# Kernel tuning notes

Hardware: AMD Instinct MI355X
Metric: run time of the kernel (lower is better)

Reference implementation:

```python
import jax, jax.numpy as jnp
import numpy as np

N_NODES = 50000
N_EDGES = 800000
D_FEAT = 96
HIDDEN = 96
AVG_DEG = 16.0


def setup_inputs() -> dict:
    key = jax.random.key(0)
    k1, k2, k3, k4, k5 = jax.random.split(key, 5)
    x = jax.random.normal(k1, (N_NODES, D_FEAT), dtype=jnp.float32)
    row = jax.random.randint(k2, (N_EDGES,), 0, N_NODES)
    col = jax.random.randint(k3, (N_EDGES,), 0, N_NODES)
    edge_index = jnp.stack([row, col]).astype(jnp.int32)  # [2, E]
    # normalized adjacency values ~ 1/degree scale
    edge_weight = jax.random.uniform(k4, (N_EDGES,), dtype=jnp.float32) / AVG_DEG
    # init_w: small normal + identity (random=False path)
    W = 0.1 * jax.random.normal(k5, (D_FEAT, HIDDEN), dtype=jnp.float32) + jnp.eye(D_FEAT, HIDDEN, dtype=jnp.float32)
    b = jnp.zeros((HIDDEN,), dtype=jnp.float32)
    return {"x": x, "W": W, "b": b, "edge_index": edge_index, "edge_weight": edge_weight}


def reference(x, W, b, edge_index, edge_weight):
    # dense projection + bias
    h = x @ W + b  # [N, H]
    # sparse adj matmul: out[i] = sum_e w_e * h[col_e] for row_e == i
    row, col = edge_index[0], edge_index[1]
    msgs = edge_weight[:, None] * h[col]  # [E, H]
    pre_nonlinearity = jax.ops.segment_sum(msgs, row, num_segments=N_NODES)  # [N, H]
    # inference path: no dropout (training=None)
    output = jax.nn.elu(pre_nonlinearity)
    return (pre_nonlinearity, output)
```

## Files before the change

### kernel.cpp

```cpp
#include <hip/hip_runtime.h>


#define D 96
#define CG 24
#define BSHIFT 6
#define BROWS 64
#define CAP 1536
#define CPAD 16
#define EB_CHUNK 3200
#define GR 64
#define XPITCH 25

typedef unsigned long long u64;
typedef unsigned short u16;
typedef unsigned int u32;

__device__ __forceinline__ u16 f2bf(float f) {
  const u32 u = __float_as_uint(f);
  return (u16)((u + 0x7FFFu + ((u >> 16) & 1u)) >> 16);
}
__device__ __forceinline__ float bf2f(u16 s) {
  return __uint_as_float(((u32)s) << 16);
}

struct ushort4_t { u16 x, y, z, w; };

__global__ __launch_bounds__(256) void init_bcur_kernel(int* __restrict__ bcur, int nbkt) {
  const int b = blockIdx.x * 256 + threadIdx.x;
  if (b < nbkt) bcur[b * CPAD] = b * CAP;
}

union FusedSmem {
  float4 sX[GR * XPITCH];
  struct { int cnt[1024]; int cur[1024]; } bz;
};

__global__ __launch_bounds__(256) void fused_gemm_bucketize(
    const float* __restrict__ x, const float4* __restrict__ W4,
    const float* __restrict__ bias, u16* __restrict__ h16, int n_nodes,
    const int* __restrict__ rows, const int* __restrict__ cols,
    const float* __restrict__ ew, int* __restrict__ bcur,
    u64* __restrict__ tmp, int n_edges, int nbkt, int bb) {
  __shared__ FusedSmem sm;
  const int tid = threadIdx.x;

  if ((int)blockIdx.x < bb) {
    for (int i = tid; i < 1024; i += 256) sm.bz.cnt[i] = 0;
    __syncthreads();
    const int e0 = blockIdx.x * EB_CHUNK;
    const int e1 = min(e0 + EB_CHUNK, n_edges);
    for (int e = e0 + tid; e < e1; e += 256)
      atomicAdd(&sm.bz.cnt[rows[e] >> BSHIFT], 1);
    __syncthreads();
    for (int b = tid; b < nbkt; b += 256) {
      const int c = sm.bz.cnt[b];
      sm.bz.cur[b] = (c > 0) ? atomicAdd(&bcur[b * CPAD], c) : 0;
    }
    __syncthreads();
    for (int e = e0 + tid; e < e1; e += 256) {
      const int r = rows[e];
      const int b = r >> BSHIFT;
      const u64 u = ((u64)__float_as_uint(ew[e]) << 32) |
                    ((u64)(r & (BROWS - 1)) << 20) | (u64)(unsigned)cols[e];
      const int pos = atomicAdd(&sm.bz.cur[b], 1);
      if (pos < (b + 1) * CAP) tmp[pos] = u;
    }
  } else {
    const int row0 = ((int)blockIdx.x - bb) * GR;
    for (int i = tid; i < GR * CG; i += 256) {
      const int r = i / CG, c = i % CG;
      float4 v = make_float4(0.f, 0.f, 0.f, 0.f);
      const int gr = row0 + r;
      if (gr < n_nodes) v = ((const float4*)x)[(size_t)gr * CG + c];
      sm.sX[r * XPITCH + c] = v;
    }
    __syncthreads();
    if (tid < 192) {
      const int cg = tid >> 3;
      const int rq = tid & 7;
      float4 acc[8];
      const float4 bv = ((const float4*)bias)[cg];
#pragma unroll
      for (int j = 0; j < 8; ++j) acc[j] = bv;

#define FMA4(A, XS, WV) \
  A.x = fmaf(XS, WV.x, A.x); A.y = fmaf(XS, WV.y, A.y); \
  A.z = fmaf(XS, WV.z, A.z); A.w = fmaf(XS, WV.w, A.w);

      for (int kb = 0; kb < 24; ++kb) {
        const float4 w0 = W4[(kb * 4 + 0) * CG + cg];
        const float4 w1 = W4[(kb * 4 + 1) * CG + cg];
        const float4 w2 = W4[(kb * 4 + 2) * CG + cg];
        const float4 w3 = W4[(kb * 4 + 3) * CG + cg];
#pragma unroll
        for (int j = 0; j < 8; ++j) {
          const float4 xv = sm.sX[(rq + 8 * j) * XPITCH + kb];
          FMA4(acc[j], xv.x, w0);
          FMA4(acc[j], xv.y, w1);
          FMA4(acc[j], xv.z, w2);
          FMA4(acc[j], xv.w, w3);
        }
      }
#pragma unroll
      for (int j = 0; j < 8; ++j) {
        const int r = row0 + rq + 8 * j;
        if (r < n_nodes) {
          ushort4_t o;
          o.x = f2bf(acc[j].x); o.y = f2bf(acc[j].y);
          o.z = f2bf(acc[j].z); o.w = f2bf(acc[j].w);
          ((ushort4_t*)h16)[(size_t)r * CG + cg] = o;
        }
      }
    }
  }
}

__global__ __launch_bounds__(256) void bucket_gather_kernel(
    const int* __restrict__ bcur, const u64* __restrict__ tmp,
    const u16* __restrict__ h16, float* __restrict__ pre,
    float* __restrict__ out, int n_nodes) {
  __shared__ u64 se[CAP];
  __shared__ int cnt[BROWS];
  __shared__ int off[BROWS + 1];
  __shared__ int cur[BROWS];
  const int tid = threadIdx.x;
  const int b = blockIdx.x;
  if (tid < BROWS) cnt[tid] = 0;
  __syncthreads();

  const int base = b * CAP;
  int count = bcur[b * CPAD] - base;
  if (count > CAP) count = CAP;

  for (int k = tid; k < count; k += 256)
    atomicAdd(&cnt[(int)((tmp[base + k] >> 20) & (BROWS - 1))], 1);
  __syncthreads();

  if (tid < BROWS) off[tid + 1] = cnt[tid];
  if (tid == 0) off[0] = 0;
  __syncthreads();
  for (int d = 1; d <= BROWS; d <<= 1) {
    int v = 0;
    if (tid <= BROWS && tid >= d) v = off[tid - d];
    __syncthreads();
    if (tid <= BROWS) off[tid] += v;
    __syncthreads();
  }
  if (tid < BROWS) cur[tid] = off[tid];
  __syncthreads();

  for (int k = tid; k < count; k += 256) {
    const u64 u = tmp[base + k];
    const int rl = (int)((u >> 20) & (BROWS - 1));
    se[atomicAdd(&cur[rl], 1)] = u;
  }
  __syncthreads();

  const int g = tid >> 5;
  const int lane = tid & 31;
  const int row0 = b * BROWS;
#pragma unroll
  for (int j = 0; j < 8; ++j) {
    const int r = g * 8 + j;
    const int row = row0 + r;
    const int s = off[r], e = off[r + 1];
    float a0 = 0.f, a1 = 0.f, a2 = 0.f;
    int k = s;
    for (; k + 1 < e; k += 2) {
      const u64 u0 = se[k], u1 = se[k + 1];
      const int c0 = (int)(u0 & 0xFFFFF), c1 = (int)(u1 & 0xFFFFF);
      const float w0 = __uint_as_float((u32)(u0 >> 32));
      const float w1 = __uint_as_float((u32)(u1 >> 32));
      const u16* h0 = h16 + (size_t)c0 * D;
      const u16* h1 = h16 + (size_t)c1 * D;
      const float p00 = bf2f(h0[lane]), p01 = bf2f(h0[lane + 32]), p02 = bf2f(h0[lane + 64]);
      const float p10 = bf2f(h1[lane]), p11 = bf2f(h1[lane + 32]), p12 = bf2f(h1[lane + 64]);
      a0 = fmaf(w0, p00, a0); a1 = fmaf(w0, p01, a1); a2 = fmaf(w0, p02, a2);
      a0 = fmaf(w1, p10, a0); a1 = fmaf(w1, p11, a1); a2 = fmaf(w1, p12, a2);
    }
    if (k < e) {
      const u64 u = se[k];
      const int c = (int)(u & 0xFFFFF);
      const float w = __uint_as_float((u32)(u >> 32));
      const u16* hr = h16 + (size_t)c * D;
      a0 = fmaf(w, bf2f(hr[lane]), a0);
      a1 = fmaf(w, bf2f(hr[lane + 32]), a1);
      a2 = fmaf(w, bf2f(hr[lane + 64]), a2);
    }
    if (row < n_nodes) {
      float* pr = pre + (size_t)row * D;
      float* orow = out + (size_t)row * D;
      pr[lane] = a0; pr[lane + 32] = a1; pr[lane + 64] = a2;
      orow[lane]      = a0 > 0.f ? a0 : (__expf(a0) - 1.f);
      orow[lane + 32] = a1 > 0.f ? a1 : (__expf(a1) - 1.f);
      orow[lane + 64] = a2 > 0.f ? a2 : (__expf(a2) - 1.f);
    }
  }
}

extern "C" void kernel_launch(void* const* d_in, const int* in_sizes, int n_in,
                              void* d_out, int out_size, void* d_ws, size_t ws_size,
                              hipStream_t stream) {
  const float* x  = (const float*)d_in[0];
  const float* W  = (const float*)d_in[1];
  const float* b  = (const float*)d_in[2];
  const int*   ei = (const int*)d_in[3];
  const float* ew = (const float*)d_in[4];

  const int n_nodes = in_sizes[0] / D;
  const int n_edges = in_sizes[4];
  const int* rows = ei;
  const int* cols = ei + n_edges;

  float* pre  = (float*)d_out;
  float* outp = pre + (size_t)n_nodes * D;

  const int nbkt = (n_nodes + BROWS - 1) / BROWS;

  char* ws = (char*)d_ws;
  u16*  h16  = (u16*)ws;   ws += (size_t)n_nodes * D * sizeof(u16);
  int*  bcur = (int*)ws;   ws += (size_t)nbkt * CPAD * sizeof(int);
  u64*  tmp  = (u64*)ws;

  init_bcur_kernel<<<(nbkt + 255) / 256, 256, 0, stream>>>(bcur, nbkt);

  const int gb = (n_nodes + GR - 1) / GR;
  const int bb = (n_edges + EB_CHUNK - 1) / EB_CHUNK;
  fused_gemm_bucketize<<<gb + bb, 256, 0, stream>>>(
      x, (const float4*)W, b, h16, n_nodes,
      rows, cols, ew, bcur, tmp, n_edges, nbkt, bb);

  bucket_gather_kernel<<<nbkt, 256, 0, stream>>>(bcur, tmp, h16, pre, outp, n_nodes);
}
```

Baseline: 155.1 us.

## Halve bucket size, stage bucket edges in LDS, unroll gather by four

Bucket width drops from 64 to 32 rows (capacity 768), so there are about twice as many gather blocks, each holding fewer edges. The shared-memory histogram in the bucketize phase grows to 1600 bins to cover the larger bucket count. The gather kernel now reads each bucket's packed edges from global memory once into an LDS staging array instead of twice. The per-row edge loop is unrolled by four to keep more independent h16 loads in flight. The costs are more LDS per block, more global atomics per edge chunk, and larger shared zero-init and per-bucket loops in the bucketize blocks.

```diff
diff --git a/kernel.cpp b/kernel.cpp
--- a/kernel.cpp
+++ b/kernel.cpp
@@ -3,11 +3,12 @@
 
 #define D 96
 #define CG 24
-#define BSHIFT 6
-#define BROWS 64
-#define CAP 1536
+#define BSHIFT 5
+#define BROWS 32
+#define CAP 768
 #define CPAD 16
 #define EB_CHUNK 3200
+#define NBKT_MAX 1600
 #define GR 64
 #define XPITCH 25
 
@@ -32,7 +33,7 @@
 
 union FusedSmem {
   float4 sX[GR * XPITCH];
-  struct { int cnt[1024]; int cur[1024]; } bz;
+  struct { int cnt[NBKT_MAX]; int cur[NBKT_MAX]; } bz;
 };
 
 __global__ __launch_bounds__(256) void fused_gemm_bucketize(
@@ -45,7 +46,7 @@
   const int tid = threadIdx.x;
 
   if ((int)blockIdx.x < bb) {
-    for (int i = tid; i < 1024; i += 256) sm.bz.cnt[i] = 0;
+    for (int i = tid; i < NBKT_MAX; i += 256) sm.bz.cnt[i] = 0;
     __syncthreads();
     const int e0 = blockIdx.x * EB_CHUNK;
     const int e1 = min(e0 + EB_CHUNK, n_edges);
@@ -119,6 +120,7 @@
     const int* __restrict__ bcur, const u64* __restrict__ tmp,
     const u16* __restrict__ h16, float* __restrict__ pre,
     float* __restrict__ out, int n_nodes) {
+  __shared__ u64 raw[CAP];
   __shared__ u64 se[CAP];
   __shared__ int cnt[BROWS];
   __shared__ int off[BROWS + 1];
@@ -132,8 +134,11 @@
   int count = bcur[b * CPAD] - base;
   if (count > CAP) count = CAP;
 
-  for (int k = tid; k < count; k += 256)
-    atomicAdd(&cnt[(int)((tmp[base + k] >> 20) & (BROWS - 1))], 1);
+  for (int k = tid; k < count; k += 256) {
+    const u64 u = tmp[base + k];
+    raw[k] = u;
+    atomicAdd(&cnt[(int)((u >> 20) & (BROWS - 1))], 1);
+  }
   __syncthreads();
 
   if (tid < BROWS) off[tid + 1] = cnt[tid];
@@ -150,7 +155,7 @@
   __syncthreads();
 
   for (int k = tid; k < count; k += 256) {
-    const u64 u = tmp[base + k];
+    const u64 u = raw[k];
     const int rl = (int)((u >> 20) & (BROWS - 1));
     se[atomicAdd(&cur[rl], 1)] = u;
   }
@@ -160,29 +165,35 @@
   const int lane = tid & 31;
   const int row0 = b * BROWS;
 #pragma unroll
-  for (int j = 0; j < 8; ++j) {
-    const int r = g * 8 + j;
+  for (int j = 0; j < 4; ++j) {
+    const int r = g * 4 + j;
     const int row = row0 + r;
     const int s = off[r], e = off[r + 1];
     float a0 = 0.f, a1 = 0.f, a2 = 0.f;
     int k = s;
-    for (; k + 1 < e; k += 2) {
-      const u64 u0 = se[k], u1 = se[k + 1];
-      const int c0 = (int)(u0 & 0xFFFFF), c1 = (int)(u1 & 0xFFFFF);
+    for (; k + 3 < e; k += 4) {
+      const u64 u0 = se[k], u1 = se[k + 1], u2 = se[k + 2], u3 = se[k + 3];
+      const u16* h0 = h16 + (size_t)(u0 & 0xFFFFF) * D;
+      const u16* h1 = h16 + (size_t)(u1 & 0xFFFFF) * D;
+      const u16* h2 = h16 + (size_t)(u2 & 0xFFFFF) * D;
+      const u16* h3 = h16 + (size_t)(u3 & 0xFFFFF) * D;
       const float w0 = __uint_as_float((u32)(u0 >> 32));
       const float w1 = __uint_as_float((u32)(u1 >> 32));
-      const u16* h0 = h16 + (size_t)c0 * D;
-      const u16* h1 = h16 + (size_t)c1 * D;
+      const float w2 = __uint_as_float((u32)(u2 >> 32));
+      const float w3 = __uint_as_float((u32)(u3 >> 32));
       const float p00 = bf2f(h0[lane]), p01 = bf2f(h0[lane + 32]), p02 = bf2f(h0[lane + 64]);
       const float p10 = bf2f(h1[lane]), p11 = bf2f(h1[lane + 32]), p12 = bf2f(h1[lane + 64]);
+      const float p20 = bf2f(h2[lane]), p21 = bf2f(h2[lane + 32]), p22 = bf2f(h2[lane + 64]);
+      const float p30 = bf2f(h3[lane]), p31 = bf2f(h3[lane + 32]), p32 = bf2f(h3[lane + 64]);
       a0 = fmaf(w0, p00, a0); a1 = fmaf(w0, p01, a1); a2 = fmaf(w0, p02, a2);
       a0 = fmaf(w1, p10, a0); a1 = fmaf(w1, p11, a1); a2 = fmaf(w1, p12, a2);
-    }
-    if (k < e) {
+      a0 = fmaf(w2, p20, a0); a1 = fmaf(w2, p21, a1); a2 = fmaf(w2, p22, a2);
+      a0 = fmaf(w3, p30, a0); a1 = fmaf(w3, p31, a1); a2 = fmaf(w3, p32, a2);
+    }
+    for (; k < e; ++k) {
       const u64 u = se[k];
-      const int c = (int)(u & 0xFFFFF);
+      const u16* hr = h16 + (size_t)(u & 0xFFFFF) * D;
       const float w = __uint_as_float((u32)(u >> 32));
-      const u16* hr = h16 + (size_t)c * D;
       a0 = fmaf(w, bf2f(hr[lane]), a0);
       a1 = fmaf(w, bf2f(hr[lane + 32]), a1);
       a2 = fmaf(w, bf2f(hr[lane + 64]), a2);
```

New measurement: 147.4 us. -5.0%, faster.
